# Performance work log

Measured on AMD Instinct MI355X. Metric: run time of the kernel, lower is better.

The kernel has to match this reference:

```python
import jax, jax.numpy as jnp
import numpy as np

N_NODES = 50000
N_EDGES = 600000
IN_FEATS = 128
N_HIDDEN = 128
N_CLASSES = 40


def setup_inputs() -> dict:
    key = jax.random.key(0)
    ks = jax.random.split(key, 12)
    feat = jax.random.normal(ks[0], (N_NODES, IN_FEATS), dtype=jnp.float32)
    src = jax.random.randint(ks[1], (N_EDGES,), 0, N_NODES, dtype=jnp.int32)
    dst = jax.random.randint(ks[2], (N_EDGES,), 0, N_NODES, dtype=jnp.int32)
    dims = [(IN_FEATS, N_HIDDEN), (N_HIDDEN, N_HIDDEN), (N_HIDDEN, N_CLASSES)]
    params = {}
    for i, (di, do) in enumerate(dims):
        s = 1.0 / np.sqrt(di)
        params[f"w_self{i}"] = jax.random.uniform(ks[3 + 3 * i], (di, do), jnp.float32, -s, s)
        params[f"w_neigh{i}"] = jax.random.uniform(ks[4 + 3 * i], (di, do), jnp.float32, -s, s)
        params[f"b{i}"] = jnp.zeros((do,), jnp.float32)
    return dict(feat=feat, src=src, dst=dst, **params)


def _sage_layer(h, src, dst, w_self, w_neigh, b):
    # mean aggregation over in-neighbors: msg = h[src], reduce at dst
    msg_sum = jax.ops.segment_sum(h[src], dst, num_segments=N_NODES)  # [N, d]
    deg = jax.ops.segment_sum(jnp.ones((src.shape[0],), h.dtype), dst, num_segments=N_NODES)
    h_neigh = msg_sum / jnp.maximum(deg, 1.0)[:, None]
    # DGL SAGEConv(mean): out = fc_self(h) + fc_neigh(mean_neigh) + bias
    return h @ w_self + h_neigh @ w_neigh + b


def reference(feat, src, dst,
              w_self0, w_neigh0, b0,
              w_self1, w_neigh1, b1,
              w_self2, w_neigh2, b2):
    # dropout p=0.0 -> identity
    h = _sage_layer(feat, src, dst, w_self0, w_neigh0, b0)
    h = jax.nn.relu(h)
    h = _sage_layer(h, src, dst, w_self1, w_neigh1, b1)
    h = jax.nn.relu(h)
    h = _sage_layer(h, src, dst, w_self2, w_neigh2, b2)
    return h
```

## Files before the change

kernel.cpp:

```cpp
#include <hip/hip_runtime.h>

#define N_NODES 50000
#define N_EDGES 600000

typedef short bf16x8 __attribute__((ext_vector_type(8)));
typedef float f32x4  __attribute__((ext_vector_type(4)));
typedef unsigned short u16x8 __attribute__((ext_vector_type(8)));
typedef unsigned short u16x4 __attribute__((ext_vector_type(4)));

__device__ inline ushort rne_bf16(float a) {
    union { float f; unsigned u; } v; v.f = a;
    return (ushort)((v.u + 0x7FFFu + ((v.u >> 16) & 1u)) >> 16);
}
__device__ inline float bf16_to_f32(ushort h) {
    return __uint_as_float((unsigned)h << 16);
}
__device__ inline void split_bf16(float a, ushort& hi, ushort& lo) {
    hi = rne_bf16(a);
    float hv = bf16_to_f32(hi);
    lo = rne_bf16(a - hv);
}


__global__ void count_deg_kernel(const int* __restrict__ dst, int* __restrict__ deg, int ne) {
    int e = blockIdx.x * blockDim.x + threadIdx.x;
    if (e < ne) atomicAdd(&deg[dst[e]], 1);
}

__global__ __launch_bounds__(256) void block_sums_kernel(const int* __restrict__ deg,
                                                         int* __restrict__ bsum, int n) {
    __shared__ int s[256];
    int t = threadIdx.x;
    int i = blockIdx.x * 256 + t;
    s[t] = (i < n) ? deg[i] : 0;
    __syncthreads();
    #pragma unroll
    for (int d = 128; d > 0; d >>= 1) {
        if (t < d) s[t] += s[t + d];
        __syncthreads();
    }
    if (t == 0) bsum[blockIdx.x] = s[0];
}

__global__ __launch_bounds__(256) void scan_bsums_kernel(const int* __restrict__ bsum,
                                                         int* __restrict__ base, int nb,
                                                         int* __restrict__ off, int n) {
    __shared__ int s[256];
    int t = threadIdx.x;
    int v = (t < nb) ? bsum[t] : 0;
    s[t] = v;
    __syncthreads();
    #pragma unroll
    for (int d = 1; d < 256; d <<= 1) {
        int x = (t >= d) ? s[t - d] : 0;
        __syncthreads();
        s[t] += x;
        __syncthreads();
    }
    if (t < nb) base[t] = s[t] - v;
    if (t == 255) off[n] = s[255];
}

__global__ __launch_bounds__(256) void scatter_offsets_kernel(const int* __restrict__ deg,
                                                              const int* __restrict__ base,
                                                              int* __restrict__ off,
                                                              int* __restrict__ cur, int n) {
    __shared__ int s[256];
    int t = threadIdx.x;
    int i = blockIdx.x * 256 + t;
    int v = (i < n) ? deg[i] : 0;
    s[t] = v;
    __syncthreads();
    #pragma unroll
    for (int d = 1; d < 256; d <<= 1) {
        int x = (t >= d) ? s[t - d] : 0;
        __syncthreads();
        s[t] += x;
        __syncthreads();
    }
    if (i < n) {
        int excl = s[t] - v + base[blockIdx.x];
        off[i] = excl;
        cur[i] = excl;
    }
}

__global__ void fill_csr_kernel(const int* __restrict__ src, const int* __restrict__ dst,
                                int* __restrict__ cur, int* __restrict__ ssrc, int ne) {
    int e = blockIdx.x * blockDim.x + threadIdx.x;
    if (e < ne) {
        int p = atomicAdd(&cur[dst[e]], 1);
        ssrc[p] = src[e];
    }
}

__global__ void convert_w_kernel(const float* __restrict__ Ws, const float* __restrict__ Wn,
                                 int dout, ushort* __restrict__ Bth, ushort* __restrict__ Btl) {
    int n = blockIdx.x;
    int k = threadIdx.x;
    float w = (n < dout) ? Ws[(long)k * dout + n] : Wn[(long)k * dout + (n - dout)];
    ushort hi, lo;
    split_bf16(w, hi, lo);
    Bth[n * 128 + k] = hi;
    Btl[n * 128 + k] = lo;
}


#define KDIM 128
#define BKC  32
#define APAD 40

__device__ inline void stage_a_tile(const float* __restrict__ A, int bm, int M, int k0,
                                    ushort* __restrict__ Ahi, ushort* __restrict__ Alo, int tid) {
    int m  = tid >> 2;
    int kq = (tid & 3) * 8;
    int grow = bm + m;
    float f[8];
    if (grow < M) {
        const float* ap = A + (long)grow * KDIM + k0 + kq;
        float4 a0 = *(const float4*)ap;
        float4 a1 = *(const float4*)(ap + 4);
        f[0] = a0.x; f[1] = a0.y; f[2] = a0.z; f[3] = a0.w;
        f[4] = a1.x; f[5] = a1.y; f[6] = a1.z; f[7] = a1.w;
    } else {
        #pragma unroll
        for (int i = 0; i < 8; ++i) f[i] = 0.f;
    }
    ushort h[8], l[8];
    #pragma unroll
    for (int i = 0; i < 8; ++i) split_bf16(f[i], h[i], l[i]);
    uint4 hw, lw;
    hw.x = (unsigned)h[0] | ((unsigned)h[1] << 16);
    hw.y = (unsigned)h[2] | ((unsigned)h[3] << 16);
    hw.z = (unsigned)h[4] | ((unsigned)h[5] << 16);
    hw.w = (unsigned)h[6] | ((unsigned)h[7] << 16);
    lw.x = (unsigned)l[0] | ((unsigned)l[1] << 16);
    lw.y = (unsigned)l[2] | ((unsigned)l[3] << 16);
    lw.z = (unsigned)l[4] | ((unsigned)l[5] << 16);
    lw.w = (unsigned)l[6] | ((unsigned)l[7] << 16);
    *(uint4*)&Ahi[m * APAD + kq] = hw;
    *(uint4*)&Alo[m * APAD + kq] = lw;
}

__global__ __launch_bounds__(256) void gemm_mfma_wide(
    const float* __restrict__ A,
    const ushort* __restrict__ Bth, const ushort* __restrict__ Btl,
    const float* __restrict__ bias,
    float* __restrict__ S, ushort* __restrict__ T, int M)
{
    __shared__ ushort Ahi[64 * APAD];
    __shared__ ushort Alo[64 * APAD];

    const int tid = threadIdx.x;
    const int bm = blockIdx.x * 64;
    const int wave = tid >> 6;
    const int lane = tid & 63;
    const int lane16 = lane & 15;
    const int quad = lane >> 4;
    const int colbase = wave * 64;

    f32x4 acc[4][4] = {};

    for (int c = 0; c < 4; ++c) {
        int k0 = c * BKC;
        __syncthreads();
        stage_a_tile(A, bm, M, k0, Ahi, Alo, tid);
        __syncthreads();

        bf16x8 ah[4], al[4];
        #pragma unroll
        for (int r = 0; r < 4; ++r) {
            int off = (16 * r + lane16) * APAD + quad * 8;
            ah[r] = *(const bf16x8*)&Ahi[off];
            al[r] = *(const bf16x8*)&Alo[off];
        }
        #pragma unroll
        for (int ct = 0; ct < 4; ++ct) {
            int col = colbase + 16 * ct + lane16;
            long boff = (long)col * KDIM + k0 + quad * 8;
            bf16x8 bh = *(const bf16x8*)(Bth + boff);
            bf16x8 bl = *(const bf16x8*)(Btl + boff);
            #pragma unroll
            for (int r = 0; r < 4; ++r) {
                acc[r][ct] = __builtin_amdgcn_mfma_f32_16x16x32_bf16(ah[r], bh, acc[r][ct], 0, 0, 0);
                acc[r][ct] = __builtin_amdgcn_mfma_f32_16x16x32_bf16(ah[r], bl, acc[r][ct], 0, 0, 0);
                acc[r][ct] = __builtin_amdgcn_mfma_f32_16x16x32_bf16(al[r], bh, acc[r][ct], 0, 0, 0);
            }
        }
    }

    #pragma unroll
    for (int ct = 0; ct < 4; ++ct) {
        int col = colbase + 16 * ct + lane16;
        bool toS = col < 128;
        float bv = toS ? bias[col] : 0.f;
        int tcol = toS ? col : col - 128;
        #pragma unroll
        for (int r = 0; r < 4; ++r) {
            #pragma unroll
            for (int i = 0; i < 4; ++i) {
                int row = bm + 16 * r + quad * 4 + i;
                if (row < M) {
                    if (toS) S[(long)row * 128 + tcol] = acc[r][ct][i] + bv;
                    else     T[(long)row * 128 + tcol] = rne_bf16(acc[r][ct][i]);
                }
            }
        }
    }
}

__global__ __launch_bounds__(256) void gemm_mfma_narrow(
    const float* __restrict__ A,
    const ushort* __restrict__ Bth, const ushort* __restrict__ Btl,
    const float* __restrict__ bias,
    float* __restrict__ S, ushort* __restrict__ T, int M)
{
    __shared__ ushort Ahi[64 * APAD];
    __shared__ ushort Alo[64 * APAD];

    const int tid = threadIdx.x;
    const int bm = blockIdx.x * 64;
    const int wave = tid >> 6;
    const int lane = tid & 63;
    const int lane16 = lane & 15;
    const int quad = lane >> 4;

    f32x4 acc[5] = {};

    for (int c = 0; c < 4; ++c) {
        int k0 = c * BKC;
        __syncthreads();
        stage_a_tile(A, bm, M, k0, Ahi, Alo, tid);
        __syncthreads();

        int aoff = (16 * wave + lane16) * APAD + quad * 8;
        bf16x8 ah = *(const bf16x8*)&Ahi[aoff];
        bf16x8 al = *(const bf16x8*)&Alo[aoff];
        #pragma unroll
        for (int ct = 0; ct < 5; ++ct) {
            int col = 16 * ct + lane16;
            long boff = (long)col * KDIM + k0 + quad * 8;
            bf16x8 bh = *(const bf16x8*)(Bth + boff);
            bf16x8 bl = *(const bf16x8*)(Btl + boff);
            acc[ct] = __builtin_amdgcn_mfma_f32_16x16x32_bf16(ah, bh, acc[ct], 0, 0, 0);
            acc[ct] = __builtin_amdgcn_mfma_f32_16x16x32_bf16(ah, bl, acc[ct], 0, 0, 0);
            acc[ct] = __builtin_amdgcn_mfma_f32_16x16x32_bf16(al, bh, acc[ct], 0, 0, 0);
        }
    }

    #pragma unroll
    for (int ct = 0; ct < 5; ++ct) {
        int col = 16 * ct + lane16;
        bool toS = col < 40;
        float bv = toS ? bias[col] : 0.f;
        int tcol = toS ? col : col - 40;
        #pragma unroll
        for (int i = 0; i < 4; ++i) {
            int row = bm + 16 * wave + quad * 4 + i;
            if (row < M) {
                if (toS) S[(long)row * 40 + tcol] = acc[ct][i] + bv;
                else     T[(long)row * 40 + tcol] = rne_bf16(acc[ct][i]);
            }
        }
    }
}


template <int RELU>
__global__ __launch_bounds__(256) void agg128_kernel(
    const float* __restrict__ S, const ushort* __restrict__ T,
    const int* __restrict__ off, const int* __restrict__ ssrc,
    float* __restrict__ out, int nnodes)
{
    const int node = (blockIdx.x * 256 + threadIdx.x) >> 6;
    if (node >= nnodes) return;
    const int lane = threadIdx.x & 63;
    const int slot = lane >> 4;
    const int col8 = (lane & 15) * 8;

    const int a = off[node];
    const int b = off[node + 1];

    f32x4 acc0a = {0,0,0,0}, acc0b = {0,0,0,0};
    f32x4 acc1a = {0,0,0,0}, acc1b = {0,0,0,0};

    int i = a;
    for (; i + 8 <= b; i += 8) {
        int s0 = ssrc[i + slot];
        int s1 = ssrc[i + 4 + slot];
        u16x8 v0 = *(const u16x8*)(T + (long)s0 * 128 + col8);
        u16x8 v1 = *(const u16x8*)(T + (long)s1 * 128 + col8);
        #pragma unroll
        for (int j = 0; j < 4; ++j) {
            acc0a[j] += bf16_to_f32(v0[j]);
            acc0b[j] += bf16_to_f32(v0[4 + j]);
            acc1a[j] += bf16_to_f32(v1[j]);
            acc1b[j] += bf16_to_f32(v1[4 + j]);
        }
    }
    for (; i < b; i += 4) {
        int e = i + slot;
        if (e < b) {
            int s = ssrc[e];
            u16x8 v = *(const u16x8*)(T + (long)s * 128 + col8);
            #pragma unroll
            for (int j = 0; j < 4; ++j) {
                acc0a[j] += bf16_to_f32(v[j]);
                acc0b[j] += bf16_to_f32(v[4 + j]);
            }
        }
    }
    f32x4 accA = acc0a + acc1a;
    f32x4 accB = acc0b + acc1b;

    #pragma unroll
    for (int m = 16; m <= 32; m <<= 1) {
        #pragma unroll
        for (int j = 0; j < 4; ++j) {
            accA[j] += __shfl_xor((float)accA[j], m);
            accB[j] += __shfl_xor((float)accB[j], m);
        }
    }

    if (slot == 0) {
        int deg = b - a;
        float scale = (deg > 0) ? (1.0f / (float)deg) : 0.f;
        f32x4 sA = *(const f32x4*)(S + (long)node * 128 + col8);
        f32x4 sB = *(const f32x4*)(S + (long)node * 128 + col8 + 4);
        f32x4 rA = sA + accA * scale;
        f32x4 rB = sB + accB * scale;
        if (RELU) {
            #pragma unroll
            for (int j = 0; j < 4; ++j) {
                rA[j] = fmaxf(rA[j], 0.f);
                rB[j] = fmaxf(rB[j], 0.f);
            }
        }
        *(f32x4*)(out + (long)node * 128 + col8) = rA;
        *(f32x4*)(out + (long)node * 128 + col8 + 4) = rB;
    }
}

template <int RELU>
__global__ __launch_bounds__(256) void agg40_kernel(
    const float* __restrict__ S, const ushort* __restrict__ T,
    const int* __restrict__ off, const int* __restrict__ ssrc,
    float* __restrict__ out, int nnodes)
{
    const int node = (blockIdx.x * 256 + threadIdx.x) >> 6;
    if (node >= nnodes) return;
    const int lane = threadIdx.x & 63;
    const bool active = lane < 60;
    const int slot = active ? (lane / 10) : 5;
    const int fi = lane % 10;
    const int fo = fi * 4;

    const int a = off[node];
    const int b = off[node + 1];

    f32x4 acc0 = {0,0,0,0}, acc1 = {0,0,0,0};

    int i = a;
    for (; i + 12 <= b; i += 12) {
        int s0 = ssrc[i + slot];
        int s1 = ssrc[i + 6 + slot];
        u16x4 v0 = *(const u16x4*)(T + (long)s0 * 40 + fo);
        u16x4 v1 = *(const u16x4*)(T + (long)s1 * 40 + fo);
        if (active) {
            #pragma unroll
            for (int j = 0; j < 4; ++j) {
                acc0[j] += bf16_to_f32(v0[j]);
                acc1[j] += bf16_to_f32(v1[j]);
            }
        }
    }
    for (; i < b; i += 6) {
        int e = i + slot;
        if (active && e < b) {
            int s = ssrc[e];
            u16x4 v = *(const u16x4*)(T + (long)s * 40 + fo);
            #pragma unroll
            for (int j = 0; j < 4; ++j) acc0[j] += bf16_to_f32(v[j]);
        }
    }
    f32x4 acc = acc0 + acc1;

    f32x4 tot = acc;
    #pragma unroll
    for (int d = 10; d <= 50; d += 10) {
        int srcl = fi + d;
        #pragma unroll
        for (int j = 0; j < 4; ++j) tot[j] += __shfl((float)acc[j], srcl);
    }

    if (lane < 10) {
        int deg = b - a;
        float scale = (deg > 0) ? (1.0f / (float)deg) : 0.f;
        f32x4 s4 = *(const f32x4*)(S + (long)node * 40 + fo);
        f32x4 r = s4 + tot * scale;
        if (RELU) {
            #pragma unroll
            for (int j = 0; j < 4; ++j) r[j] = fmaxf(r[j], 0.f);
        }
        *(f32x4*)(out + (long)node * 40 + fo) = r;
    }
}


extern "C" void kernel_launch(void* const* d_in, const int* in_sizes, int n_in,
                              void* d_out, int out_size, void* d_ws, size_t ws_size,
                              hipStream_t stream) {
    const float* feat = (const float*)d_in[0];
    const int*   src  = (const int*)d_in[1];
    const int*   dst  = (const int*)d_in[2];
    const float* ws0  = (const float*)d_in[3];
    const float* wn0  = (const float*)d_in[4];
    const float* b0   = (const float*)d_in[5];
    const float* ws1  = (const float*)d_in[6];
    const float* wn1  = (const float*)d_in[7];
    const float* b1   = (const float*)d_in[8];
    const float* ws2  = (const float*)d_in[9];
    const float* wn2  = (const float*)d_in[10];
    const float* b2   = (const float*)d_in[11];

    const int N = N_NODES;
    const int NE = N_EDGES;
    const int NB = (N + 255) / 256;

    char* ws = (char*)d_ws;
    int*    offsets = (int*)(ws + 0);
    int*    cursor  = (int*)(ws + 200704);
    int*    degi    = (int*)(ws + 401408);
    int*    bsum    = (int*)(ws + 601600);
    int*    bbase   = (int*)(ws + 602432);
    int*    ssrc    = (int*)(ws + 603648);
    ushort* Bth0 = (ushort*)(ws + 200704);
    ushort* Btl0 = (ushort*)(ws + 266240);
    ushort* Bth1 = (ushort*)(ws + 331776);
    ushort* Btl1 = (ushort*)(ws + 397312);
    ushort* Bth2 = (ushort*)(ws + 462848);
    ushort* Btl2 = (ushort*)(ws + 483328);
    float*  hbuf = (float*)(ws + 3003904);
    float*  sbuf = (float*)(ws + 28603904);
    ushort* tbuf = (ushort*)(ws + 54203904);

    hipMemsetAsync(degi, 0, (size_t)N * sizeof(int), stream);
    count_deg_kernel<<<(NE + 255) / 256, 256, 0, stream>>>(dst, degi, NE);
    block_sums_kernel<<<NB, 256, 0, stream>>>(degi, bsum, N);
    scan_bsums_kernel<<<1, 256, 0, stream>>>(bsum, bbase, NB, offsets, N);
    scatter_offsets_kernel<<<NB, 256, 0, stream>>>(degi, bbase, offsets, cursor, N);
    fill_csr_kernel<<<(NE + 255) / 256, 256, 0, stream>>>(src, dst, cursor, ssrc, NE);

    convert_w_kernel<<<256, 128, 0, stream>>>(ws0, wn0, 128, Bth0, Btl0);
    convert_w_kernel<<<256, 128, 0, stream>>>(ws1, wn1, 128, Bth1, Btl1);
    convert_w_kernel<<<80, 128, 0, stream>>>(ws2, wn2, 40, Bth2, Btl2);

    const int gx = (N + 63) / 64;
    const int ga = (N + 3) / 4;

    gemm_mfma_wide<<<gx, 256, 0, stream>>>(feat, Bth0, Btl0, b0, sbuf, tbuf, N);
    agg128_kernel<1><<<ga, 256, 0, stream>>>(sbuf, tbuf, offsets, ssrc, hbuf, N);

    gemm_mfma_wide<<<gx, 256, 0, stream>>>(hbuf, Bth1, Btl1, b1, sbuf, tbuf, N);
    agg128_kernel<1><<<ga, 256, 0, stream>>>(sbuf, tbuf, offsets, ssrc, hbuf, N);

    gemm_mfma_narrow<<<gx, 256, 0, stream>>>(hbuf, Bth2, Btl2, b2, sbuf, tbuf, N);
    agg40_kernel<0><<<ga, 256, 0, stream>>>(sbuf, tbuf, offsets, ssrc, (float*)d_out, N);
}
```

Measured before the change: 337.0 us.

## Load A fragments directly into registers, dropping LDS staging in GEMMs

Both GEMM kernels stop staging the fp32 A tile into shared memory as split bf16 and the associated barriers. Each lane now loads its own A fragment from global memory and splits it into hi/lo bf16 in registers. The wide GEMM also shrinks its row tile from 64 to 32 per block and doubles the grid. Each wave in the wide kernel now loads the same A rows redundantly, so global/L2 traffic and split work rise four-fold in exchange for removing syncs and LDS round-trips.

```diff
diff --git a/kernel.cpp b/kernel.cpp
--- a/kernel.cpp
+++ b/kernel.cpp
@@ -108,38 +108,18 @@
 
 #define KDIM 128
 #define BKC  32
-#define APAD 40
-
-__device__ inline void stage_a_tile(const float* __restrict__ A, int bm, int M, int k0,
-                                    ushort* __restrict__ Ahi, ushort* __restrict__ Alo, int tid) {
-    int m  = tid >> 2;
-    int kq = (tid & 3) * 8;
-    int grow = bm + m;
-    float f[8];
-    if (grow < M) {
-        const float* ap = A + (long)grow * KDIM + k0 + kq;
-        float4 a0 = *(const float4*)ap;
-        float4 a1 = *(const float4*)(ap + 4);
-        f[0] = a0.x; f[1] = a0.y; f[2] = a0.z; f[3] = a0.w;
-        f[4] = a1.x; f[5] = a1.y; f[6] = a1.z; f[7] = a1.w;
-    } else {
-        #pragma unroll
-        for (int i = 0; i < 8; ++i) f[i] = 0.f;
-    }
-    ushort h[8], l[8];
-    #pragma unroll
-    for (int i = 0; i < 8; ++i) split_bf16(f[i], h[i], l[i]);
-    uint4 hw, lw;
-    hw.x = (unsigned)h[0] | ((unsigned)h[1] << 16);
-    hw.y = (unsigned)h[2] | ((unsigned)h[3] << 16);
-    hw.z = (unsigned)h[4] | ((unsigned)h[5] << 16);
-    hw.w = (unsigned)h[6] | ((unsigned)h[7] << 16);
-    lw.x = (unsigned)l[0] | ((unsigned)l[1] << 16);
-    lw.y = (unsigned)l[2] | ((unsigned)l[3] << 16);
-    lw.z = (unsigned)l[4] | ((unsigned)l[5] << 16);
-    lw.w = (unsigned)l[6] | ((unsigned)l[7] << 16);
-    *(uint4*)&Ahi[m * APAD + kq] = hw;
-    *(uint4*)&Alo[m * APAD + kq] = lw;
+
+__device__ inline void load_split_a(const float* __restrict__ ap, bf16x8& ah, bf16x8& al) {
+    float4 a0 = *(const float4*)ap;
+    float4 a1 = *(const float4*)(ap + 4);
+    float f[8] = {a0.x, a0.y, a0.z, a0.w, a1.x, a1.y, a1.z, a1.w};
+    #pragma unroll
+    for (int i = 0; i < 8; ++i) {
+        ushort h, l;
+        split_bf16(f[i], h, l);
+        ah[i] = (short)h;
+        al[i] = (short)l;
+    }
 }
 
 __global__ __launch_bounds__(256) void gemm_mfma_wide(
@@ -148,44 +128,40 @@
     const float* __restrict__ bias,
     float* __restrict__ S, ushort* __restrict__ T, int M)
 {
-    __shared__ ushort Ahi[64 * APAD];
-    __shared__ ushort Alo[64 * APAD];
-
     const int tid = threadIdx.x;
-    const int bm = blockIdx.x * 64;
     const int wave = tid >> 6;
     const int lane = tid & 63;
     const int lane16 = lane & 15;
     const int quad = lane >> 4;
+    const int bm = blockIdx.x * 32;
     const int colbase = wave * 64;
 
-    f32x4 acc[4][4] = {};
-
+    const int row0 = bm + lane16;
+    const int row1 = row0 + 16;
+    const bool ok0 = row0 < M;
+    const bool ok1 = row1 < M;
+
+    f32x4 acc[2][4] = {};
+
+    #pragma unroll 2
     for (int c = 0; c < 4; ++c) {
-        int k0 = c * BKC;
-        __syncthreads();
-        stage_a_tile(A, bm, M, k0, Ahi, Alo, tid);
-        __syncthreads();
-
-        bf16x8 ah[4], al[4];
-        #pragma unroll
-        for (int r = 0; r < 4; ++r) {
-            int off = (16 * r + lane16) * APAD + quad * 8;
-            ah[r] = *(const bf16x8*)&Ahi[off];
-            al[r] = *(const bf16x8*)&Alo[off];
-        }
+        const int k0 = c * BKC + quad * 8;
+
+        bf16x8 ah0 = {}, al0 = {}, ah1 = {}, al1 = {};
+        if (ok0) load_split_a(A + (long)row0 * KDIM + k0, ah0, al0);
+        if (ok1) load_split_a(A + (long)row1 * KDIM + k0, ah1, al1);
+
         #pragma unroll
         for (int ct = 0; ct < 4; ++ct) {
-            int col = colbase + 16 * ct + lane16;
-            long boff = (long)col * KDIM + k0 + quad * 8;
+            const long boff = (long)(colbase + 16 * ct + lane16) * KDIM + k0;
             bf16x8 bh = *(const bf16x8*)(Bth + boff);
             bf16x8 bl = *(const bf16x8*)(Btl + boff);
-            #pragma unroll
-            for (int r = 0; r < 4; ++r) {
-                acc[r][ct] = __builtin_amdgcn_mfma_f32_16x16x32_bf16(ah[r], bh, acc[r][ct], 0, 0, 0);
-                acc[r][ct] = __builtin_amdgcn_mfma_f32_16x16x32_bf16(ah[r], bl, acc[r][ct], 0, 0, 0);
-                acc[r][ct] = __builtin_amdgcn_mfma_f32_16x16x32_bf16(al[r], bh, acc[r][ct], 0, 0, 0);
-            }
+            acc[0][ct] = __builtin_amdgcn_mfma_f32_16x16x32_bf16(ah0, bh, acc[0][ct], 0, 0, 0);
+            acc[0][ct] = __builtin_amdgcn_mfma_f32_16x16x32_bf16(ah0, bl, acc[0][ct], 0, 0, 0);
+            acc[0][ct] = __builtin_amdgcn_mfma_f32_16x16x32_bf16(al0, bh, acc[0][ct], 0, 0, 0);
+            acc[1][ct] = __builtin_amdgcn_mfma_f32_16x16x32_bf16(ah1, bh, acc[1][ct], 0, 0, 0);
+            acc[1][ct] = __builtin_amdgcn_mfma_f32_16x16x32_bf16(ah1, bl, acc[1][ct], 0, 0, 0);
+            acc[1][ct] = __builtin_amdgcn_mfma_f32_16x16x32_bf16(al1, bh, acc[1][ct], 0, 0, 0);
         }
     }
 
@@ -196,7 +172,7 @@
         float bv = toS ? bias[col] : 0.f;
         int tcol = toS ? col : col - 128;
         #pragma unroll
-        for (int r = 0; r < 4; ++r) {
+        for (int r = 0; r < 2; ++r) {
             #pragma unroll
             for (int i = 0; i < 4; ++i) {
                 int row = bm + 16 * r + quad * 4 + i;
@@ -215,31 +191,28 @@
     const float* __restrict__ bias,
     float* __restrict__ S, ushort* __restrict__ T, int M)
 {
-    __shared__ ushort Ahi[64 * APAD];
-    __shared__ ushort Alo[64 * APAD];
-
     const int tid = threadIdx.x;
-    const int bm = blockIdx.x * 64;
     const int wave = tid >> 6;
     const int lane = tid & 63;
     const int lane16 = lane & 15;
     const int quad = lane >> 4;
+    const int bm = blockIdx.x * 64 + wave * 16;
+
+    const int row0 = bm + lane16;
+    const bool ok0 = row0 < M;
 
     f32x4 acc[5] = {};
 
+    #pragma unroll 2
     for (int c = 0; c < 4; ++c) {
-        int k0 = c * BKC;
-        __syncthreads();
-        stage_a_tile(A, bm, M, k0, Ahi, Alo, tid);
-        __syncthreads();
-
-        int aoff = (16 * wave + lane16) * APAD + quad * 8;
-        bf16x8 ah = *(const bf16x8*)&Ahi[aoff];
-        bf16x8 al = *(const bf16x8*)&Alo[aoff];
+        const int k0 = c * BKC + quad * 8;
+
+        bf16x8 ah = {}, al = {};
+        if (ok0) load_split_a(A + (long)row0 * KDIM + k0, ah, al);
+
         #pragma unroll
         for (int ct = 0; ct < 5; ++ct) {
-            int col = 16 * ct + lane16;
-            long boff = (long)col * KDIM + k0 + quad * 8;
+            const long boff = (long)(16 * ct + lane16) * KDIM + k0;
             bf16x8 bh = *(const bf16x8*)(Bth + boff);
             bf16x8 bl = *(const bf16x8*)(Btl + boff);
             acc[ct] = __builtin_amdgcn_mfma_f32_16x16x32_bf16(ah, bh, acc[ct], 0, 0, 0);
@@ -256,7 +229,7 @@
         int tcol = toS ? col : col - 40;
         #pragma unroll
         for (int i = 0; i < 4; ++i) {
-            int row = bm + 16 * wave + quad * 4 + i;
+            int row = bm + quad * 4 + i;
             if (row < M) {
                 if (toS) S[(long)row * 40 + tcol] = acc[ct][i] + bv;
                 else     T[(long)row * 40 + tcol] = rne_bf16(acc[ct][i]);
@@ -455,15 +428,16 @@
     convert_w_kernel<<<256, 128, 0, stream>>>(ws1, wn1, 128, Bth1, Btl1);
     convert_w_kernel<<<80, 128, 0, stream>>>(ws2, wn2, 40, Bth2, Btl2);
 
-    const int gx = (N + 63) / 64;
+    const int gw = (N + 31) / 32;
+    const int gn = (N + 63) / 64;
     const int ga = (N + 3) / 4;
 
-    gemm_mfma_wide<<<gx, 256, 0, stream>>>(feat, Bth0, Btl0, b0, sbuf, tbuf, N);
+    gemm_mfma_wide<<<gw, 256, 0, stream>>>(feat, Bth0, Btl0, b0, sbuf, tbuf, N);
     agg128_kernel<1><<<ga, 256, 0, stream>>>(sbuf, tbuf, offsets, ssrc, hbuf, N);
 
-    gemm_mfma_wide<<<gx, 256, 0, stream>>>(hbuf, Bth1, Btl1, b1, sbuf, tbuf, N);
+    gemm_mfma_wide<<<gw, 256, 0, stream>>>(hbuf, Bth1, Btl1, b1, sbuf, tbuf, N);
     agg128_kernel<1><<<ga, 256, 0, stream>>>(sbuf, tbuf, offsets, ssrc, hbuf, N);
 
-    gemm_mfma_narrow<<<gx, 256, 0, stream>>>(hbuf, Bth2, Btl2, b2, sbuf, tbuf, N);
+    gemm_mfma_narrow<<<gn, 256, 0, stream>>>(hbuf, Bth2, Btl2, b2, sbuf, tbuf, N);
     agg40_kernel<0><<<ga, 256, 0, stream>>>(sbuf, tbuf, offsets, ssrc, (float*)d_out, N);
 }
```

Result: slower. 373.6 us (+10.9%).

## Stage full K A-tile once and swap MFMA operands for vectorized stores

Applied to the files above, without the earlier changes.

Both GEMM kernels now convert and stage the whole 64x128 A tile into LDS once with a single barrier, replacing four staged chunks with eight barriers. The MFMA operands are swapped so each lane holds four consecutive output columns of one row. That lets the epilogue write float4 and packed bf16x4 stores instead of scalar strided stores. LDS use per block grows to about 35KB, which may reduce occupancy.

```diff
diff --git a/kernel.cpp b/kernel.cpp
--- a/kernel.cpp
+++ b/kernel.cpp
@@ -107,39 +107,41 @@
 
 
 #define KDIM 128
-#define BKC  32
-#define APAD 40
-
-__device__ inline void stage_a_tile(const float* __restrict__ A, int bm, int M, int k0,
-                                    ushort* __restrict__ Ahi, ushort* __restrict__ Alo, int tid) {
-    int m  = tid >> 2;
-    int kq = (tid & 3) * 8;
-    int grow = bm + m;
-    float f[8];
-    if (grow < M) {
-        const float* ap = A + (long)grow * KDIM + k0 + kq;
-        float4 a0 = *(const float4*)ap;
-        float4 a1 = *(const float4*)(ap + 4);
-        f[0] = a0.x; f[1] = a0.y; f[2] = a0.z; f[3] = a0.w;
-        f[4] = a1.x; f[5] = a1.y; f[6] = a1.z; f[7] = a1.w;
-    } else {
-        #pragma unroll
-        for (int i = 0; i < 8; ++i) f[i] = 0.f;
-    }
-    ushort h[8], l[8];
-    #pragma unroll
-    for (int i = 0; i < 8; ++i) split_bf16(f[i], h[i], l[i]);
-    uint4 hw, lw;
-    hw.x = (unsigned)h[0] | ((unsigned)h[1] << 16);
-    hw.y = (unsigned)h[2] | ((unsigned)h[3] << 16);
-    hw.z = (unsigned)h[4] | ((unsigned)h[5] << 16);
-    hw.w = (unsigned)h[6] | ((unsigned)h[7] << 16);
-    lw.x = (unsigned)l[0] | ((unsigned)l[1] << 16);
-    lw.y = (unsigned)l[2] | ((unsigned)l[3] << 16);
-    lw.z = (unsigned)l[4] | ((unsigned)l[5] << 16);
-    lw.w = (unsigned)l[6] | ((unsigned)l[7] << 16);
-    *(uint4*)&Ahi[m * APAD + kq] = hw;
-    *(uint4*)&Alo[m * APAD + kq] = lw;
+#define APAD 136
+
+__device__ inline void stage_a_full(const float* __restrict__ A, int bm, int M, int tid,
+                                    ushort* __restrict__ Ahi, ushort* __restrict__ Alo) {
+    const int m  = tid >> 2;
+    const int kq = (tid & 3) * 32;
+    const int grow = bm + m;
+    #pragma unroll
+    for (int g = 0; g < 4; ++g) {
+        float f[8];
+        if (grow < M) {
+            const float* ap = A + (long)grow * KDIM + kq + g * 8;
+            float4 a0 = *(const float4*)ap;
+            float4 a1 = *(const float4*)(ap + 4);
+            f[0] = a0.x; f[1] = a0.y; f[2] = a0.z; f[3] = a0.w;
+            f[4] = a1.x; f[5] = a1.y; f[6] = a1.z; f[7] = a1.w;
+        } else {
+            #pragma unroll
+            for (int i = 0; i < 8; ++i) f[i] = 0.f;
+        }
+        ushort h[8], l[8];
+        #pragma unroll
+        for (int i = 0; i < 8; ++i) split_bf16(f[i], h[i], l[i]);
+        uint4 hw, lw;
+        hw.x = (unsigned)h[0] | ((unsigned)h[1] << 16);
+        hw.y = (unsigned)h[2] | ((unsigned)h[3] << 16);
+        hw.z = (unsigned)h[4] | ((unsigned)h[5] << 16);
+        hw.w = (unsigned)h[6] | ((unsigned)h[7] << 16);
+        lw.x = (unsigned)l[0] | ((unsigned)l[1] << 16);
+        lw.y = (unsigned)l[2] | ((unsigned)l[3] << 16);
+        lw.z = (unsigned)l[4] | ((unsigned)l[5] << 16);
+        lw.w = (unsigned)l[6] | ((unsigned)l[7] << 16);
+        *(uint4*)&Ahi[m * APAD + kq + g * 8] = hw;
+        *(uint4*)&Alo[m * APAD + kq + g * 8] = lw;
+    }
 }
 
 __global__ __launch_bounds__(256) void gemm_mfma_wide(
@@ -152,57 +154,59 @@
     __shared__ ushort Alo[64 * APAD];
 
     const int tid = threadIdx.x;
-    const int bm = blockIdx.x * 64;
     const int wave = tid >> 6;
     const int lane = tid & 63;
     const int lane16 = lane & 15;
     const int quad = lane >> 4;
+    const int bm = blockIdx.x * 64;
     const int colbase = wave * 64;
 
+    stage_a_full(A, bm, M, tid, Ahi, Alo);
+    __syncthreads();
+
     f32x4 acc[4][4] = {};
 
+    #pragma unroll
     for (int c = 0; c < 4; ++c) {
-        int k0 = c * BKC;
-        __syncthreads();
-        stage_a_tile(A, bm, M, k0, Ahi, Alo, tid);
-        __syncthreads();
-
+        const int k0 = c * 32 + quad * 8;
         bf16x8 ah[4], al[4];
         #pragma unroll
         for (int r = 0; r < 4; ++r) {
-            int off = (16 * r + lane16) * APAD + quad * 8;
+            int off = (16 * r + lane16) * APAD + k0;
             ah[r] = *(const bf16x8*)&Ahi[off];
             al[r] = *(const bf16x8*)&Alo[off];
         }
         #pragma unroll
         for (int ct = 0; ct < 4; ++ct) {
-            int col = colbase + 16 * ct + lane16;
-            long boff = (long)col * KDIM + k0 + quad * 8;
+            const long boff = (long)(colbase + 16 * ct + lane16) * KDIM + k0;
             bf16x8 bh = *(const bf16x8*)(Bth + boff);
             bf16x8 bl = *(const bf16x8*)(Btl + boff);
             #pragma unroll
             for (int r = 0; r < 4; ++r) {
-                acc[r][ct] = __builtin_amdgcn_mfma_f32_16x16x32_bf16(ah[r], bh, acc[r][ct], 0, 0, 0);
-                acc[r][ct] = __builtin_amdgcn_mfma_f32_16x16x32_bf16(ah[r], bl, acc[r][ct], 0, 0, 0);
-                acc[r][ct] = __builtin_amdgcn_mfma_f32_16x16x32_bf16(al[r], bh, acc[r][ct], 0, 0, 0);
+                acc[r][ct] = __builtin_amdgcn_mfma_f32_16x16x32_bf16(bh, ah[r], acc[r][ct], 0, 0, 0);
+                acc[r][ct] = __builtin_amdgcn_mfma_f32_16x16x32_bf16(bl, ah[r], acc[r][ct], 0, 0, 0);
+                acc[r][ct] = __builtin_amdgcn_mfma_f32_16x16x32_bf16(bh, al[r], acc[r][ct], 0, 0, 0);
             }
         }
     }
 
     #pragma unroll
     for (int ct = 0; ct < 4; ++ct) {
-        int col = colbase + 16 * ct + lane16;
-        bool toS = col < 128;
-        float bv = toS ? bias[col] : 0.f;
-        int tcol = toS ? col : col - 128;
+        const int col0 = colbase + 16 * ct + quad * 4;
+        const bool toS = col0 < 128;
+        f32x4 bv = {0,0,0,0};
+        if (toS) bv = *(const f32x4*)(bias + col0);
         #pragma unroll
         for (int r = 0; r < 4; ++r) {
-            #pragma unroll
-            for (int i = 0; i < 4; ++i) {
-                int row = bm + 16 * r + quad * 4 + i;
-                if (row < M) {
-                    if (toS) S[(long)row * 128 + tcol] = acc[r][ct][i] + bv;
-                    else     T[(long)row * 128 + tcol] = rne_bf16(acc[r][ct][i]);
+            const int row = bm + 16 * r + lane16;
+            if (row < M) {
+                if (toS) {
+                    *(f32x4*)(S + (long)row * 128 + col0) = acc[r][ct] + bv;
+                } else {
+                    u16x4 t4;
+                    #pragma unroll
+                    for (int i = 0; i < 4; ++i) t4[i] = rne_bf16(acc[r][ct][i]);
+                    *(u16x4*)(T + (long)row * 128 + (col0 - 128)) = t4;
                 }
             }
         }
@@ -219,47 +223,48 @@
     __shared__ ushort Alo[64 * APAD];
 
     const int tid = threadIdx.x;
-    const int bm = blockIdx.x * 64;
     const int wave = tid >> 6;
     const int lane = tid & 63;
     const int lane16 = lane & 15;
     const int quad = lane >> 4;
+    const int bm = blockIdx.x * 64;
+
+    stage_a_full(A, bm, M, tid, Ahi, Alo);
+    __syncthreads();
 
     f32x4 acc[5] = {};
 
+    #pragma unroll
     for (int c = 0; c < 4; ++c) {
-        int k0 = c * BKC;
-        __syncthreads();
-        stage_a_tile(A, bm, M, k0, Ahi, Alo, tid);
-        __syncthreads();
-
-        int aoff = (16 * wave + lane16) * APAD + quad * 8;
-        bf16x8 ah = *(const bf16x8*)&Ahi[aoff];
-        bf16x8 al = *(const bf16x8*)&Alo[aoff];
+        const int k0 = c * 32 + quad * 8;
+        const int off = (16 * wave + lane16) * APAD + k0;
+        bf16x8 ah = *(const bf16x8*)&Ahi[off];
+        bf16x8 al = *(const bf16x8*)&Alo[off];
         #pragma unroll
         for (int ct = 0; ct < 5; ++ct) {
-            int col = 16 * ct + lane16;
-            long boff = (long)col * KDIM + k0 + quad * 8;
+            const long boff = (long)(16 * ct + lane16) * KDIM + k0;
             bf16x8 bh = *(const bf16x8*)(Bth + boff);
             bf16x8 bl = *(const bf16x8*)(Btl + boff);
-            acc[ct] = __builtin_amdgcn_mfma_f32_16x16x32_bf16(ah, bh, acc[ct], 0, 0, 0);
-            acc[ct] = __builtin_amdgcn_mfma_f32_16x16x32_bf16(ah, bl, acc[ct], 0, 0, 0);
-            acc[ct] = __builtin_amdgcn_mfma_f32_16x16x32_bf16(al, bh, acc[ct], 0, 0, 0);
+            acc[ct] = __builtin_amdgcn_mfma_f32_16x16x32_bf16(bh, ah, acc[ct], 0, 0, 0);
+            acc[ct] = __builtin_amdgcn_mfma_f32_16x16x32_bf16(bl, ah, acc[ct], 0, 0, 0);
+            acc[ct] = __builtin_amdgcn_mfma_f32_16x16x32_bf16(bh, al, acc[ct], 0, 0, 0);
         }
     }
 
     #pragma unroll
     for (int ct = 0; ct < 5; ++ct) {
-        int col = 16 * ct + lane16;
-        bool toS = col < 40;
-        float bv = toS ? bias[col] : 0.f;
-        int tcol = toS ? col : col - 40;
-        #pragma unroll
-        for (int i = 0; i < 4; ++i) {
-            int row = bm + 16 * wave + quad * 4 + i;
-            if (row < M) {
-                if (toS) S[(long)row * 40 + tcol] = acc[ct][i] + bv;
-                else     T[(long)row * 40 + tcol] = rne_bf16(acc[ct][i]);
+        const int col0 = 16 * ct + quad * 4;
+        const bool toS = col0 < 40;
+        const int row = bm + 16 * wave + lane16;
+        if (row < M) {
+            if (toS) {
+                f32x4 bv = *(const f32x4*)(bias + col0);
+                *(f32x4*)(S + (long)row * 40 + col0) = acc[ct] + bv;
+            } else {
+                u16x4 t4;
+                #pragma unroll
+                for (int i = 0; i < 4; ++i) t4[i] = rne_bf16(acc[ct][i]);
+                *(u16x4*)(T + (long)row * 40 + (col0 - 40)) = t4;
             }
         }
     }
```

After: 340.3 us. Within noise of the previous version (+1.0%).
